# Kernel optimization log

Hardware: AMD Instinct MI355X
Metric: run time of the kernel (lower is better)

The kernel has to match this reference:

```python
import jax, jax.numpy as jnp
import numpy as np

C = 256   # hidden_size (in_channels)
V = 97    # VOC_SIZE + 1
T = 32    # encoder time steps
N = 4096  # batch of text instances


def setup_inputs() -> dict:
    key = jax.random.key(0)
    ks = jax.random.split(key, 10)
    s = lambda k, shape: jax.random.normal(k, shape, dtype=jnp.float32) * 0.05
    return {
        "input": jax.random.randint(ks[0], (N,), 0, V),
        "hidden": s(ks[1], (1, N, C)),
        "encoder_outputs": s(ks[2], (T, N, C)),
        "emb": s(ks[3], (V, C)),
        "combine_w": s(ks[4], (C, 2 * C)), "combine_b": jnp.zeros((C,), jnp.float32),
        "vat_w": s(ks[5], (1, C)), "vat_b": jnp.zeros((1,), jnp.float32),
        "gru_w_ih": s(ks[6], (3 * C, C)), "gru_w_hh": s(ks[7], (3 * C, C)),
        "gru_b_ih": jnp.zeros((3 * C,), jnp.float32), "gru_b_hh": jnp.zeros((3 * C,), jnp.float32),
        "out_w": s(ks[8], (V, C)), "out_b": jnp.zeros((V,), jnp.float32),
    }


def reference(input, hidden, encoder_outputs, emb, combine_w, combine_b,
              vat_w, vat_b, gru_w_ih, gru_w_hh, gru_b_ih, gru_b_hh,
              out_w, out_b):
    # Embedding lookup (dropout = identity in eval mode)
    embedded = emb[input]                                   # [N, C]

    # Bahdanau additive attention: vat(tanh(hidden + enc))
    alpha = jnp.tanh(hidden + encoder_outputs)              # [T, N, C]
    scores = jnp.einsum('tnc,c->nt', alpha, vat_w[0]) + vat_b[0]  # [N, T]
    attn = jax.nn.softmax(scores, axis=1)                   # [N, T]
    applied = jnp.einsum('nt,tnc->nc', attn, encoder_outputs)     # [N, C]

    # Combine + relu
    x = jnp.concatenate([embedded, applied], axis=1) @ combine_w.T + combine_b  # [N, C]
    x = jax.nn.relu(x)

    # Single-step GRU cell (PyTorch gate ordering: r, z, n)
    h = hidden[0]                                           # [N, C]
    gi = x @ gru_w_ih.T + gru_b_ih                          # [N, 3C]
    gh = h @ gru_w_hh.T + gru_b_hh                          # [N, 3C]
    ir, iz, i_n = jnp.split(gi, 3, axis=1)
    hr, hz, h_n = jnp.split(gh, 3, axis=1)
    r = jax.nn.sigmoid(ir + hr)
    z = jax.nn.sigmoid(iz + hz)
    n = jnp.tanh(i_n + r * h_n)
    h_new = (1.0 - z) * n + z * h                           # [N, C]

    out = jax.nn.log_softmax(h_new @ out_w.T + out_b, axis=1)  # [N, V]
    return out, h_new[None, :, :], attn[:, None, :]
```

## Files before the change

kernel.cpp:

```cpp
#include <hip/hip_runtime.h>

typedef unsigned short u16;
typedef unsigned int u32;
using bf16x8 = __attribute__((ext_vector_type(8))) __bf16;
using f32x4  = __attribute__((ext_vector_type(4))) float;

__device__ __forceinline__ u16 f2bf(float f) {
  union { float f; unsigned int i; } v; v.f = f;
  unsigned int r = v.i + 0x7fffu + ((v.i >> 16) & 1u);
  return (u16)(r >> 16);
}
__device__ __forceinline__ void cvt8(u16* dst, const float* src) {
  float4 a0 = *reinterpret_cast<const float4*>(src);
  float4 a1 = *reinterpret_cast<const float4*>(src + 4);
  dst[0] = f2bf(a0.x); dst[1] = f2bf(a0.y); dst[2] = f2bf(a0.z); dst[3] = f2bf(a0.w);
  dst[4] = f2bf(a1.x); dst[5] = f2bf(a1.y); dst[6] = f2bf(a1.z); dst[7] = f2bf(a1.w);
}
__device__ __forceinline__ float ftanh(float x) {
  float e = __expf(2.f * x);
  return 1.f - 2.f / (e + 1.f);
}
__device__ __forceinline__ float fsigm(float x) {
  return 1.f / (1.f + __expf(-x));
}
__device__ __forceinline__ float ptanh(float x) {
  const float c1 = -0.3333333333f, c2 = 0.1333333333f, c3 = -0.0539682540f;
  float t = x * x;
  float r = __builtin_fmaf(__builtin_fmaf(c3, t, c2), t, c1);
  return __builtin_fmaf(x * t, r, x);
}

__global__ __launch_bounds__(256) void k_score(
    const float* __restrict__ enc, const float* __restrict__ hid,
    const float* __restrict__ vw, float* __restrict__ sc)
{
  const int tid = threadIdx.x;
  const int lane = tid & 63;
  const int wave = tid >> 6;
  const int pair = blockIdx.x * 4 + wave;
  const int n = pair & 4095;

  const float4 e4 = *reinterpret_cast<const float4*>(&enc[(size_t)pair * 256 + lane * 4]);
  const float4 h4 = *reinterpret_cast<const float4*>(&hid[n * 256 + lane * 4]);
  const float4 w4 = *reinterpret_cast<const float4*>(&vw[lane * 4]);

  float s = ptanh(h4.x + e4.x) * w4.x;
  s = __builtin_fmaf(ptanh(h4.y + e4.y), w4.y, s);
  s = __builtin_fmaf(ptanh(h4.z + e4.z), w4.z, s);
  s = __builtin_fmaf(ptanh(h4.w + e4.w), w4.w, s);

  #pragma unroll
  for (int k = 32; k >= 1; k >>= 1) s += __shfl_xor(s, k, 64);
  if (lane == 0) sc[pair] = s;
}

__global__ __launch_bounds__(256) void k_apply(
    const float* __restrict__ enc, const float* __restrict__ sc,
    const float* __restrict__ emb, const int* __restrict__ inp,
    float* __restrict__ attn_out, u16* __restrict__ Acomb)
{
  __shared__ float a_s[32];

  const int n = blockIdx.x;
  const int tid = threadIdx.x;

  if (tid < 32) {
    float s = sc[tid * 4096 + n];
    float m = s;
    #pragma unroll
    for (int k = 16; k >= 1; k >>= 1) m = fmaxf(m, __shfl_xor(m, k, 64));
    float e = __expf(s - m);
    float sum = e;
    #pragma unroll
    for (int k = 16; k >= 1; k >>= 1) sum += __shfl_xor(sum, k, 64);
    float a = e / sum;
    a_s[tid] = a;
    attn_out[n * 32 + tid] = a;
  }
  __syncthreads();

  const float* base = enc + (size_t)n * 256 + tid;
  float ac0 = 0.f, ac1 = 0.f, ac2 = 0.f, ac3 = 0.f;
  #pragma unroll
  for (int t = 0; t < 32; t += 4) {
    float v0 = base[(size_t)(t + 0) * 1048576];
    float v1 = base[(size_t)(t + 1) * 1048576];
    float v2 = base[(size_t)(t + 2) * 1048576];
    float v3 = base[(size_t)(t + 3) * 1048576];
    ac0 = __builtin_fmaf(a_s[t + 0], v0, ac0);
    ac1 = __builtin_fmaf(a_s[t + 1], v1, ac1);
    ac2 = __builtin_fmaf(a_s[t + 2], v2, ac2);
    ac3 = __builtin_fmaf(a_s[t + 3], v3, ac3);
  }
  Acomb[n * 512 + 256 + tid] = f2bf((ac0 + ac1) + (ac2 + ac3));
  Acomb[n * 512 + tid] = f2bf(emb[inp[n] * 256 + tid]);
}

__global__ __launch_bounds__(256) void k_combine(
    const u16* __restrict__ A, const float* __restrict__ W,
    const float* __restrict__ bias, u16* __restrict__ X)
{
  __shared__ u16 As[64 * 40];
  __shared__ u16 Bs[64 * 40];

  const int tid = threadIdx.x;
  const int lane = tid & 63;
  const int wave = tid >> 6;
  const int lr = lane & 15, quad = lane >> 4;
  const int m0 = blockIdx.x * 64;
  const int j0 = blockIdx.y * 64;
  const int wm = (wave & 1) * 32;
  const int wn = (wave >> 1) * 32;
  const int sr = tid >> 2, sq = tid & 3;

  f32x4 acc[2][2] = {};

  for (int kt = 0; kt < 16; ++kt) {
    int k0 = kt * 32;
    *reinterpret_cast<uint4*>(&As[sr * 40 + sq * 8]) =
      *reinterpret_cast<const uint4*>(&A[(m0 + sr) * 512 + k0 + sq * 8]);
    cvt8(&Bs[sr * 40 + sq * 8], &W[(j0 + sr) * 512 + k0 + sq * 8]);
    __syncthreads();
    bf16x8 aF[2], bF[2];
    #pragma unroll
    for (int s = 0; s < 2; ++s) {
      aF[s] = *reinterpret_cast<const bf16x8*>(&As[(wm + s * 16 + lr) * 40 + quad * 8]);
      bF[s] = *reinterpret_cast<const bf16x8*>(&Bs[(wn + s * 16 + lr) * 40 + quad * 8]);
    }
    #pragma unroll
    for (int sm = 0; sm < 2; ++sm)
      #pragma unroll
      for (int sn = 0; sn < 2; ++sn)
        acc[sm][sn] = __builtin_amdgcn_mfma_f32_16x16x32_bf16(aF[sm], bF[sn], acc[sm][sn], 0, 0, 0);
    __syncthreads();
  }

  #pragma unroll
  for (int sm = 0; sm < 2; ++sm) {
    #pragma unroll
    for (int sn = 0; sn < 2; ++sn) {
      int gc = j0 + wn + sn * 16 + lr;
      float bv = bias[gc];
      int gr = m0 + wm + sm * 16 + quad * 4;
      #pragma unroll
      for (int r = 0; r < 4; ++r) {
        float v = acc[sm][sn][r] + bv;
        X[(gr + r) * 256 + gc] = f2bf(fmaxf(v, 0.f));
      }
    }
  }
}

__global__ __launch_bounds__(256) void k_gru(
    const u16* __restrict__ X, const float* __restrict__ Hin,
    const float* __restrict__ Wih, const float* __restrict__ Whh,
    const float* __restrict__ bih, const float* __restrict__ bhh,
    float* __restrict__ Hout)
{
  __shared__ u16 Xs[64 * 40];
  __shared__ u16 Hs[64 * 40];
  __shared__ u16 Bs[6 * 32 * 40];

  const int tid = threadIdx.x;
  const int lane = tid & 63;
  const int wave = tid >> 6;
  const int lr = lane & 15, quad = lane >> 4;
  const int m0 = blockIdx.x * 64;
  const int c0 = blockIdx.y * 32;

  f32x4 aI[3][2] = {};
  f32x4 aH[3][2] = {};

  for (int kt = 0; kt < 8; ++kt) {
    int k0 = kt * 32;
    for (int ci = tid; ci < 1280; ci += 256) {
      if (ci < 256) {
        int r = ci >> 2, q = ci & 3;
        *reinterpret_cast<uint4*>(&Xs[r * 40 + q * 8]) =
          *reinterpret_cast<const uint4*>(&X[(m0 + r) * 256 + k0 + q * 8]);
      } else if (ci < 512) {
        int b = ci - 256;
        int r = b >> 2, q = b & 3;
        cvt8(&Hs[r * 40 + q * 8], &Hin[(m0 + r) * 256 + k0 + q * 8]);
      } else {
        int b = ci - 512;
        int g = b >> 7, r = (b >> 2) & 31, q = b & 3;
        const float* Wsrc = (g < 3) ? Wih : Whh;
        int gg = (g < 3) ? g : g - 3;
        cvt8(&Bs[(g * 32 + r) * 40 + q * 8],
             &Wsrc[(gg * 256 + c0 + r) * 256 + k0 + q * 8]);
      }
    }
    __syncthreads();
    bf16x8 xF = *reinterpret_cast<const bf16x8*>(&Xs[(wave * 16 + lr) * 40 + quad * 8]);
    bf16x8 hF = *reinterpret_cast<const bf16x8*>(&Hs[(wave * 16 + lr) * 40 + quad * 8]);
    #pragma unroll
    for (int g = 0; g < 3; ++g) {
      #pragma unroll
      for (int sn = 0; sn < 2; ++sn) {
        bf16x8 bI = *reinterpret_cast<const bf16x8*>(&Bs[(g * 32 + sn * 16 + lr) * 40 + quad * 8]);
        bf16x8 bH = *reinterpret_cast<const bf16x8*>(&Bs[((g + 3) * 32 + sn * 16 + lr) * 40 + quad * 8]);
        aI[g][sn] = __builtin_amdgcn_mfma_f32_16x16x32_bf16(xF, bI, aI[g][sn], 0, 0, 0);
        aH[g][sn] = __builtin_amdgcn_mfma_f32_16x16x32_bf16(hF, bH, aH[g][sn], 0, 0, 0);
      }
    }
    __syncthreads();
  }

  #pragma unroll
  for (int sn = 0; sn < 2; ++sn) {
    int gc = c0 + sn * 16 + lr;
    float b_ir = bih[gc],       b_hr = bhh[gc];
    float b_iz = bih[256 + gc], b_hz = bhh[256 + gc];
    float b_in = bih[512 + gc], b_hn = bhh[512 + gc];
    #pragma unroll
    for (int r = 0; r < 4; ++r) {
      int grow = m0 + wave * 16 + quad * 4 + r;
      float rg = fsigm(aI[0][sn][r] + b_ir + aH[0][sn][r] + b_hr);
      float zg = fsigm(aI[1][sn][r] + b_iz + aH[1][sn][r] + b_hz);
      float ng = ftanh(aI[2][sn][r] + b_in + rg * (aH[2][sn][r] + b_hn));
      float hv = Hin[grow * 256 + gc];
      Hout[grow * 256 + gc] = (1.f - zg) * ng + zg * hv;
    }
  }
}

__global__ __launch_bounds__(256) void k_out(
    const float* __restrict__ H, const float* __restrict__ Wo,
    const float* __restrict__ bo, float* __restrict__ O)
{
  __shared__ u16 As[32 * 40];
  __shared__ u16 Bs[128 * 40];
  __shared__ float L[32 * 101];
  __shared__ float pm[32 * 8], pl[32 * 8];
  __shared__ float lz_s[32];

  const int tid = threadIdx.x;
  const int lane = tid & 63;
  const int wave = tid >> 6;
  const int lr = lane & 15, quad = lane >> 4;
  const int m0 = blockIdx.x * 32;
  const int rg = (wave >> 1) * 16;
  const int sg = (wave & 1) * 4;

  for (int i = tid; i < 128 * 40; i += 256) { if ((i / 40) >= 97) Bs[i] = 0; }

  f32x4 acc[4] = {};

  for (int kt = 0; kt < 8; ++kt) {
    int k0 = kt * 32;
    if (tid < 128) {
      int r = tid >> 2, q = tid & 3;
      cvt8(&As[r * 40 + q * 8], &H[(m0 + r) * 256 + k0 + q * 8]);
    }
    #pragma unroll
    for (int it = 0; it < 2; ++it) {
      int ci = tid + it * 256;
      int br = ci >> 2, bq = ci & 3;
      if (br < 97)
        cvt8(&Bs[br * 40 + bq * 8], &Wo[br * 256 + k0 + bq * 8]);
    }
    __syncthreads();
    bf16x8 aF = *reinterpret_cast<const bf16x8*>(&As[(rg + lr) * 40 + quad * 8]);
    #pragma unroll
    for (int s = 0; s < 4; ++s) {
      bf16x8 bF = *reinterpret_cast<const bf16x8*>(&Bs[((sg + s) * 16 + lr) * 40 + quad * 8]);
      acc[s] = __builtin_amdgcn_mfma_f32_16x16x32_bf16(aF, bF, acc[s], 0, 0, 0);
    }
    __syncthreads();
  }

  #pragma unroll
  for (int s = 0; s < 4; ++s) {
    int col = (sg + s) * 16 + lr;
    if (col < 97) {
      float bv = bo[col];
      #pragma unroll
      for (int r = 0; r < 4; ++r)
        L[(rg + quad * 4 + r) * 101 + col] = acc[s][r] + bv;
    }
  }
  __syncthreads();

  {
    int row = tid >> 3, p = tid & 7;
    float m = -1e30f, l = 0.f;
    for (int c = p; c < 97; c += 8) {
      float v = L[row * 101 + c];
      if (v > m) { l = l * __expf(m - v) + 1.f; m = v; }
      else l += __expf(v - m);
    }
    pm[row * 8 + p] = m; pl[row * 8 + p] = l;
  }
  __syncthreads();

  if (tid < 32) {
    float M = -1e30f;
    #pragma unroll
    for (int p = 0; p < 8; ++p) M = fmaxf(M, pm[tid * 8 + p]);
    float S = 0.f;
    #pragma unroll
    for (int p = 0; p < 8; ++p) S += pl[tid * 8 + p] * __expf(pm[tid * 8 + p] - M);
    lz_s[tid] = M + __logf(S);
  }
  __syncthreads();

  {
    int row = tid >> 3, p = tid & 7;
    float lz = lz_s[row];
    for (int c = p; c < 97; c += 8)
      O[(m0 + row) * 97 + c] = L[row * 101 + c] - lz;
  }
}

extern "C" void kernel_launch(void* const* d_in, const int* in_sizes, int n_in,
                              void* d_out, int out_size, void* d_ws, size_t ws_size,
                              hipStream_t stream) {
  const int*   inp = (const int*)d_in[0];
  const float* hid = (const float*)d_in[1];
  const float* enc = (const float*)d_in[2];
  const float* emb = (const float*)d_in[3];
  const float* cw  = (const float*)d_in[4];
  const float* cb  = (const float*)d_in[5];
  const float* vw  = (const float*)d_in[6];
  const float* wih = (const float*)d_in[8];
  const float* whh = (const float*)d_in[9];
  const float* bih = (const float*)d_in[10];
  const float* bhh = (const float*)d_in[11];
  const float* ow  = (const float*)d_in[12];
  const float* ob  = (const float*)d_in[13];

  float* out        = (float*)d_out;
  float* out_logits = out;
  float* out_h      = out + 4096 * 97;
  float* out_attn   = out_h + 4096 * 256;

  u16* Acomb = (u16*)d_ws;
  u16* Xbuf  = Acomb + 4096 * 512;
  float* Sc  = (float*)(Xbuf + 4096 * 256);

  k_score<<<32768, 256, 0, stream>>>(enc, hid, vw, Sc);
  k_apply<<<4096, 256, 0, stream>>>(enc, Sc, emb, inp, out_attn, Acomb);
  k_combine<<<dim3(64, 4), 256, 0, stream>>>(Acomb, cw, cb, Xbuf);
  k_gru<<<dim3(64, 8), 256, 0, stream>>>(Xbuf, hid, wih, whh, bih, bhh, out_h);
  k_out<<<128, 256, 0, stream>>>(out_h, ow, ob, out_logits);
}
```

Baseline: 302.7 us.

## Fuse attention scoring and context application into one online-softmax kernel

Merges the score and apply kernels so each encoder element is read once. The softmax normalizer is accumulated alongside the context. Drops the max subtraction in softmax, relying on small score magnitudes. Uses 16 batch rows per 512-thread block with 8 channels per thread, giving far fewer blocks. Removes the intermediate score buffer and one launch.

```diff
diff --git a/kernel.cpp b/kernel.cpp
--- a/kernel.cpp
+++ b/kernel.cpp
@@ -30,70 +30,79 @@
   return __builtin_fmaf(x * t, r, x);
 }
 
-__global__ __launch_bounds__(256) void k_score(
+__global__ __launch_bounds__(512) void k_attn(
     const float* __restrict__ enc, const float* __restrict__ hid,
-    const float* __restrict__ vw, float* __restrict__ sc)
-{
-  const int tid = threadIdx.x;
-  const int lane = tid & 63;
-  const int wave = tid >> 6;
-  const int pair = blockIdx.x * 4 + wave;
-  const int n = pair & 4095;
-
-  const float4 e4 = *reinterpret_cast<const float4*>(&enc[(size_t)pair * 256 + lane * 4]);
-  const float4 h4 = *reinterpret_cast<const float4*>(&hid[n * 256 + lane * 4]);
-  const float4 w4 = *reinterpret_cast<const float4*>(&vw[lane * 4]);
-
-  float s = ptanh(h4.x + e4.x) * w4.x;
-  s = __builtin_fmaf(ptanh(h4.y + e4.y), w4.y, s);
-  s = __builtin_fmaf(ptanh(h4.z + e4.z), w4.z, s);
-  s = __builtin_fmaf(ptanh(h4.w + e4.w), w4.w, s);
-
-  #pragma unroll
-  for (int k = 32; k >= 1; k >>= 1) s += __shfl_xor(s, k, 64);
-  if (lane == 0) sc[pair] = s;
-}
-
-__global__ __launch_bounds__(256) void k_apply(
-    const float* __restrict__ enc, const float* __restrict__ sc,
+    const float* __restrict__ vw,
     const float* __restrict__ emb, const int* __restrict__ inp,
     float* __restrict__ attn_out, u16* __restrict__ Acomb)
 {
-  __shared__ float a_s[32];
-
-  const int n = blockIdx.x;
+  __shared__ float es_s[16 * 33];
+  __shared__ float l_s[16];
+
   const int tid = threadIdx.x;
-
-  if (tid < 32) {
-    float s = sc[tid * 4096 + n];
-    float m = s;
-    #pragma unroll
-    for (int k = 16; k >= 1; k >>= 1) m = fmaxf(m, __shfl_xor(m, k, 64));
-    float e = __expf(s - m);
-    float sum = e;
-    #pragma unroll
-    for (int k = 16; k >= 1; k >>= 1) sum += __shfl_xor(sum, k, 64);
-    float a = e / sum;
-    a_s[tid] = a;
-    attn_out[n * 32 + tid] = a;
-  }
+  const int nl  = tid >> 5;
+  const int cg  = tid & 31;
+  const int c0  = cg * 8;
+  const int n   = blockIdx.x * 16 + nl;
+
+  const float4 h0 = *reinterpret_cast<const float4*>(&hid[n * 256 + c0]);
+  const float4 h1 = *reinterpret_cast<const float4*>(&hid[n * 256 + c0 + 4]);
+  const float4 w0 = *reinterpret_cast<const float4*>(&vw[c0]);
+  const float4 w1 = *reinterpret_cast<const float4*>(&vw[c0 + 4]);
+
+  float a0=0.f,a1=0.f,a2=0.f,a3=0.f,a4=0.f,a5=0.f,a6=0.f,a7=0.f;
+  float l = 0.f;
+
+  const float* ep = &enc[(size_t)n * 256 + c0];
+  #pragma unroll 4
+  for (int t = 0; t < 32; ++t) {
+    const float* p = ep + (size_t)t * 1048576;
+    float4 e0 = *reinterpret_cast<const float4*>(p);
+    float4 e1 = *reinterpret_cast<const float4*>(p + 4);
+
+    float s;
+    s  = ptanh(h0.x + e0.x) * w0.x;
+    s  = __builtin_fmaf(ptanh(h0.y + e0.y), w0.y, s);
+    s  = __builtin_fmaf(ptanh(h0.z + e0.z), w0.z, s);
+    s  = __builtin_fmaf(ptanh(h0.w + e0.w), w0.w, s);
+    s  = __builtin_fmaf(ptanh(h1.x + e1.x), w1.x, s);
+    s  = __builtin_fmaf(ptanh(h1.y + e1.y), w1.y, s);
+    s  = __builtin_fmaf(ptanh(h1.z + e1.z), w1.z, s);
+    s  = __builtin_fmaf(ptanh(h1.w + e1.w), w1.w, s);
+    #pragma unroll
+    for (int k = 16; k >= 1; k >>= 1) s += __shfl_xor(s, k, 64);
+
+    float e = __expf(s);
+    l += e;
+    a0 = __builtin_fmaf(e, e0.x, a0); a1 = __builtin_fmaf(e, e0.y, a1);
+    a2 = __builtin_fmaf(e, e0.z, a2); a3 = __builtin_fmaf(e, e0.w, a3);
+    a4 = __builtin_fmaf(e, e1.x, a4); a5 = __builtin_fmaf(e, e1.y, a5);
+    a6 = __builtin_fmaf(e, e1.z, a6); a7 = __builtin_fmaf(e, e1.w, a7);
+    if (cg == 0) es_s[nl * 33 + t] = e;
+  }
+
+  {
+    float rl = 1.f / l;
+    u16 tmp[8];
+    tmp[0]=f2bf(a0*rl); tmp[1]=f2bf(a1*rl); tmp[2]=f2bf(a2*rl); tmp[3]=f2bf(a3*rl);
+    tmp[4]=f2bf(a4*rl); tmp[5]=f2bf(a5*rl); tmp[6]=f2bf(a6*rl); tmp[7]=f2bf(a7*rl);
+    *reinterpret_cast<uint4*>(&Acomb[n * 512 + 256 + c0]) =
+      *reinterpret_cast<const uint4*>(tmp);
+  }
+  {
+    int row = inp[n];
+    u16 tmp[8];
+    cvt8(tmp, &emb[row * 256 + c0]);
+    *reinterpret_cast<uint4*>(&Acomb[n * 512 + c0]) =
+      *reinterpret_cast<const uint4*>(tmp);
+  }
+  if (cg == 0) l_s[nl] = l;
   __syncthreads();
 
-  const float* base = enc + (size_t)n * 256 + tid;
-  float ac0 = 0.f, ac1 = 0.f, ac2 = 0.f, ac3 = 0.f;
-  #pragma unroll
-  for (int t = 0; t < 32; t += 4) {
-    float v0 = base[(size_t)(t + 0) * 1048576];
-    float v1 = base[(size_t)(t + 1) * 1048576];
-    float v2 = base[(size_t)(t + 2) * 1048576];
-    float v3 = base[(size_t)(t + 3) * 1048576];
-    ac0 = __builtin_fmaf(a_s[t + 0], v0, ac0);
-    ac1 = __builtin_fmaf(a_s[t + 1], v1, ac1);
-    ac2 = __builtin_fmaf(a_s[t + 2], v2, ac2);
-    ac3 = __builtin_fmaf(a_s[t + 3], v3, ac3);
-  }
-  Acomb[n * 512 + 256 + tid] = f2bf((ac0 + ac1) + (ac2 + ac3));
-  Acomb[n * 512 + tid] = f2bf(emb[inp[n] * 256 + tid]);
+  {
+    int n2 = tid >> 5, t2 = tid & 31;
+    attn_out[(blockIdx.x * 16 + n2) * 32 + t2] = es_s[n2 * 33 + t2] / l_s[n2];
+  }
 }
 
 __global__ __launch_bounds__(256) void k_combine(
@@ -337,10 +346,8 @@
 
   u16* Acomb = (u16*)d_ws;
   u16* Xbuf  = Acomb + 4096 * 512;
-  float* Sc  = (float*)(Xbuf + 4096 * 256);
-
-  k_score<<<32768, 256, 0, stream>>>(enc, hid, vw, Sc);
-  k_apply<<<4096, 256, 0, stream>>>(enc, Sc, emb, inp, out_attn, Acomb);
+
+  k_attn<<<256, 512, 0, stream>>>(enc, hid, vw, emb, inp, out_attn, Acomb);
   k_combine<<<dim3(64, 4), 256, 0, stream>>>(Acomb, cw, cb, Xbuf);
   k_gru<<<dim3(64, 8), 256, 0, stream>>>(Xbuf, hid, wih, whh, bih, bhh, out_h);
   k_out<<<128, 256, 0, stream>>>(out_h, ow, ob, out_logits);
```

Result: faster. 276.7 us (-8.6%).
